# Performance work log

Measured on AMD Instinct MI355X. Metric: run time of the kernel, lower is better.

## Reference

```python
import jax, jax.numpy as jnp
import numpy as np

B, C, N = 16, 3, 4096
K = 20
IN_CH, HID, OUT_CH = 2 * C, 64, 64
EPS = 1e-5
NEG_SLOPE = 0.2


def setup_inputs() -> dict:
    key = jax.random.key(0)
    ks = jax.random.split(key, 4)
    return {
        "x": jax.random.normal(ks[0], (B, C, N), dtype=jnp.float32),
        "W1": jax.random.normal(ks[1], (HID, IN_CH), dtype=jnp.float32) * 0.1,
        "W2": jax.random.normal(ks[2], (HID, HID), dtype=jnp.float32) * 0.1,
        "W3": jax.random.normal(ks[3], (OUT_CH, HID), dtype=jnp.float32) * 0.1,
        "g1": jnp.ones((HID,), jnp.float32),
        "b1": jnp.zeros((HID,), jnp.float32),
        "g2": jnp.ones((OUT_CH,), jnp.float32),
        "b2": jnp.zeros((OUT_CH,), jnp.float32),
    }


def _lrelu(y):
    return jnp.where(y > 0, y, NEG_SLOPE * y)


def _bn(y, gamma, beta):
    # training-mode BatchNorm2d: stats over all axes except channel (last here)
    mu = jnp.mean(y, axis=(0, 1, 2), keepdims=True)
    var = jnp.mean((y - mu) ** 2, axis=(0, 1, 2), keepdims=True)
    return (y - mu) * jax.lax.rsqrt(var + EPS) * gamma + beta


def _graph_feature(x, k):
    # x: [B, C, N] -> DGCNN edge features [B, N, k, 2C]
    xt = jnp.transpose(x, (0, 2, 1))  # [B, N, C]
    sq = jnp.sum(xt * xt, axis=-1)    # [B, N]
    # negative squared pairwise distance (top_k picks nearest, incl. self)
    neg_dist = 2.0 * jnp.einsum('bnc,bmc->bnm', xt, xt) - sq[:, :, None] - sq[:, None, :]
    _, idx = jax.lax.top_k(neg_dist, k)                 # [B, N, k]
    nbr = jax.vmap(lambda xb, ib: xb[ib])(xt, idx)      # [B, N, k, C] gather
    xc = jnp.broadcast_to(xt[:, :, None, :], nbr.shape)
    return jnp.concatenate([nbr - xc, xc], axis=-1)     # [B, N, k, 2C]


def reference(x, W1, W2, W3, g1, b1, g2, b2):
    f = _graph_feature(x, K)                    # [B, N, k, 2C]
    # 1x1 convs over channel axis (last), matching NCHW permute(0,3,2,1)
    y = jnp.einsum('bnkc,oc->bnko', f, W1)
    y = _bn(_lrelu(y), g1, b1)
    y = jnp.einsum('bnkc,oc->bnko', y, W2)
    y = _bn(_lrelu(y), g1, b1)                  # norm1 is reused (shared params)
    y = jnp.einsum('bnkc,oc->bnko', y, W3)
    y = _bn(_lrelu(y), g2, b2)
    y = jnp.max(y, axis=2)                      # max over k neighbors -> [B, N, out]
    return jnp.transpose(y, (0, 2, 1))          # [B, out, N]
```

## Files before the change

kernel.cpp:

```cpp
#include <hip/hip_runtime.h>
#include <math.h>

#define KNN 20
#define CNT_INV (1.0f / 1310720.0f)

typedef short bf16x8 __attribute__((ext_vector_type(8)));
typedef float f32x4  __attribute__((ext_vector_type(4)));

__device__ __forceinline__ short f2bf(float f) {
  unsigned u = __builtin_bit_cast(unsigned, f);
  u += 0x7FFFu + ((u >> 16) & 1u);
  return (short)(u >> 16);
}
__device__ __forceinline__ float lrelu(float y) { return y > 0.f ? y : 0.2f * y; }

__global__ __launch_bounds__(256) void xt4_kernel(const float* __restrict__ x,
                                                  float4* __restrict__ xt4) {
  const int t = blockIdx.x * 256 + threadIdx.x;
  const int b = t >> 12, m = t & 4095;
  const float* xb = x + (size_t)b * 12288;
  const float a = xb[m], c = xb[4096 + m], e = xb[8192 + m];
  xt4[t] = make_float4(a, c, e, a * a + c * c + e * e);
}

__global__ __launch_bounds__(256) void knn_kernel(const float4* __restrict__ xt4,
                                                  int* __restrict__ idx_out,
                                                  const float* __restrict__ W1,
                                                  float* __restrict__ s1buf) {
  __shared__ __align__(16) int hist[1024];
  __shared__ int sB[8];
  __shared__ int wcnt[4][4];
  __shared__ int slist[4][64];
  __shared__ int scnt[4];
  __shared__ int eidx[4][KNN];
  const int tid = threadIdx.x, lane = tid & 63, wid = tid >> 6;
  const int p0 = blockIdx.x * 4;
  const int b = p0 >> 12, n0 = p0 & 4095;
  const float4* xb4 = xt4 + (size_t)b * 4096;
  const float4 cp0 = xb4[n0], cp1 = xb4[n0 + 1], cp2 = xb4[n0 + 2], cp3 = xb4[n0 + 3];

  float w1r[6];
#pragma unroll
  for (int c = 0; c < 6; ++c) w1r[c] = W1[lane * 6 + c];

  float d0[16], d1[16], d2[16], d3[16];
#pragma unroll
  for (int i = 0; i < 16; ++i) {
    const float4 qv = xb4[i * 256 + tid];
    const float t0 = fmaf(cp0.x, qv.x, fmaf(cp0.y, qv.y, cp0.z * qv.z));
    const float t1 = fmaf(cp1.x, qv.x, fmaf(cp1.y, qv.y, cp1.z * qv.z));
    const float t2 = fmaf(cp2.x, qv.x, fmaf(cp2.y, qv.y, cp2.z * qv.z));
    const float t3 = fmaf(cp3.x, qv.x, fmaf(cp3.y, qv.y, cp3.z * qv.z));
    d0[i] = fmaf(-2.0f, t0, qv.w) + cp0.w;
    d1[i] = fmaf(-2.0f, t1, qv.w) + cp1.w;
    d2[i] = fmaf(-2.0f, t2, qv.w) + cp2.w;
    d3[i] = fmaf(-2.0f, t3, qv.w) + cp3.w;
  }

  *(int4*)&hist[tid * 4] = int4{0, 0, 0, 0};
  __syncthreads();
#pragma unroll
  for (int i = 0; i < 16; ++i) {
    if (d0[i] < 2.0f) atomicAdd(&hist[      (int)(d0[i] * 128.0f)], 1);
    if (d1[i] < 2.0f) atomicAdd(&hist[256 + (int)(d1[i] * 128.0f)], 1);
    if (d2[i] < 2.0f) atomicAdd(&hist[512 + (int)(d2[i] * 128.0f)], 1);
    if (d3[i] < 2.0f) atomicAdd(&hist[768 + (int)(d3[i] * 128.0f)], 1);
  }
  __syncthreads();
  {
    const int* h = &hist[wid * 256];
    int Bv = 256, cntv = 0, seam = 0;
#pragma unroll
    for (int c = 0; c < 4; ++c) {
      if (Bv == 256) {
        int s = h[c * 64 + lane];
#pragma unroll
        for (int off = 1; off < 64; off <<= 1) { const int t = __shfl_up(s, off); if (lane >= off) s += t; }
        s += seam;
        const unsigned long long m = __ballot(s >= 20);
        if (m) { const int l = __ffsll((long long)m) - 1; Bv = c * 64 + l; cntv = __shfl(s, l); }
        else seam = __shfl(s, 63);
      }
    }
    if (lane == 0) { sB[wid * 2] = Bv; sB[wid * 2 + 1] = cntv; }
  }
  __syncthreads();

  float lo0 = 0.f, R0 = 2.f, lo1 = 0.f, R1 = 2.f, lo2 = 0.f, R2 = 2.f, lo3 = 0.f, R3 = 2.f;
  int bef0 = 0, bef1 = 0, bef2 = 0, bef3 = 0;
  float Dedge0 = 1e30f, Dedge1 = 1e30f, Dedge2 = 1e30f, Dedge3 = 1e30f;
  bool dn0 = false, dn1 = false, dn2 = false, dn3 = false;
  {
    const float bw = 2.0f * (1.0f / 256.0f);
    bool zm0 = false, zm1 = false, zm2 = false, zm3 = false;
    {
      const int Bq = sB[0], cq = sB[1];
      if (Bq == 256) R0 = 32.0f;
      else {
        Dedge0 = (float)(Bq + 1) * bw;
        if (cq <= 48) dn0 = true;
        else { lo0 = (float)Bq * bw; R0 = bw; zm0 = true; }
      }
    }
    {
      const int Bq = sB[2], cq = sB[3];
      if (Bq == 256) R1 = 32.0f;
      else {
        Dedge1 = (float)(Bq + 1) * bw;
        if (cq <= 48) dn1 = true;
        else { lo1 = (float)Bq * bw; R1 = bw; zm1 = true; }
      }
    }
    {
      const int Bq = sB[4], cq = sB[5];
      if (Bq == 256) R2 = 32.0f;
      else {
        Dedge2 = (float)(Bq + 1) * bw;
        if (cq <= 48) dn2 = true;
        else { lo2 = (float)Bq * bw; R2 = bw; zm2 = true; }
      }
    }
    {
      const int Bq = sB[6], cq = sB[7];
      if (Bq == 256) R3 = 32.0f;
      else {
        Dedge3 = (float)(Bq + 1) * bw;
        if (cq <= 48) dn3 = true;
        else { lo3 = (float)Bq * bw; R3 = bw; zm3 = true; }
      }
    }
    if (zm0) {
      int c = 0;
#pragma unroll
      for (int i = 0; i < 16; ++i) c += (int)__popcll(__ballot(d0[i] < lo0));
      if (lane == 0) wcnt[0][wid] = c;
    }
    if (zm1) {
      int c = 0;
#pragma unroll
      for (int i = 0; i < 16; ++i) c += (int)__popcll(__ballot(d1[i] < lo1));
      if (lane == 0) wcnt[1][wid] = c;
    }
    if (zm2) {
      int c = 0;
#pragma unroll
      for (int i = 0; i < 16; ++i) c += (int)__popcll(__ballot(d2[i] < lo2));
      if (lane == 0) wcnt[2][wid] = c;
    }
    if (zm3) {
      int c = 0;
#pragma unroll
      for (int i = 0; i < 16; ++i) c += (int)__popcll(__ballot(d3[i] < lo3));
      if (lane == 0) wcnt[3][wid] = c;
    }
    if (zm0 | zm1 | zm2 | zm3) {
      __syncthreads();
      if (zm0) bef0 = wcnt[0][0] + wcnt[0][1] + wcnt[0][2] + wcnt[0][3];
      if (zm1) bef1 = wcnt[1][0] + wcnt[1][1] + wcnt[1][2] + wcnt[1][3];
      if (zm2) bef2 = wcnt[2][0] + wcnt[2][1] + wcnt[2][2] + wcnt[2][3];
      if (zm3) bef3 = wcnt[3][0] + wcnt[3][1] + wcnt[3][2] + wcnt[3][3];
    }
  }

  for (int pass = 1; pass < 6 && !(dn0 && dn1 && dn2 && dn3); ++pass) {
    *(int4*)&hist[tid * 4] = int4{0, 0, 0, 0};
    __syncthreads();
    const float sc0 = 256.0f / R0, sc1 = 256.0f / R1;
    const float sc2 = 256.0f / R2, sc3 = 256.0f / R3;
    if (!dn0) {
#pragma unroll
      for (int i = 0; i < 16; ++i) {
        const float rel = d0[i] - lo0;
        if (rel >= 0.0f && rel < R0) {
          int bin = (int)(rel * sc0); bin = bin > 255 ? 255 : bin;
          atomicAdd(&hist[bin], 1);
        }
      }
    }
    if (!dn1) {
#pragma unroll
      for (int i = 0; i < 16; ++i) {
        const float rel = d1[i] - lo1;
        if (rel >= 0.0f && rel < R1) {
          int bin = (int)(rel * sc1); bin = bin > 255 ? 255 : bin;
          atomicAdd(&hist[256 + bin], 1);
        }
      }
    }
    if (!dn2) {
#pragma unroll
      for (int i = 0; i < 16; ++i) {
        const float rel = d2[i] - lo2;
        if (rel >= 0.0f && rel < R2) {
          int bin = (int)(rel * sc2); bin = bin > 255 ? 255 : bin;
          atomicAdd(&hist[512 + bin], 1);
        }
      }
    }
    if (!dn3) {
#pragma unroll
      for (int i = 0; i < 16; ++i) {
        const float rel = d3[i] - lo3;
        if (rel >= 0.0f && rel < R3) {
          int bin = (int)(rel * sc3); bin = bin > 255 ? 255 : bin;
          atomicAdd(&hist[768 + bin], 1);
        }
      }
    }
    __syncthreads();
    {
      const bool skip = wid == 0 ? dn0 : wid == 1 ? dn1 : wid == 2 ? dn2 : dn3;
      if (!skip) {
        const int* h = &hist[wid * 256];
        int s0 = h[lane], s1 = h[64 + lane], s2 = h[128 + lane], s3 = h[192 + lane];
#pragma unroll
        for (int off = 1; off < 64; off <<= 1) { const int t = __shfl_up(s0, off); if (lane >= off) s0 += t; }
#pragma unroll
        for (int off = 1; off < 64; off <<= 1) { const int t = __shfl_up(s1, off); if (lane >= off) s1 += t; }
#pragma unroll
        for (int off = 1; off < 64; off <<= 1) { const int t = __shfl_up(s2, off); if (lane >= off) s2 += t; }
#pragma unroll
        for (int off = 1; off < 64; off <<= 1) { const int t = __shfl_up(s3, off); if (lane >= off) s3 += t; }
        s1 += __shfl(s0, 63);
        s2 += __shfl(s1, 63);
        s3 += __shfl(s2, 63);
        const int bef = wid == 0 ? bef0 : wid == 1 ? bef1 : wid == 2 ? bef2 : bef3;
        s0 += bef; s1 += bef; s2 += bef; s3 += bef;
        int B = 256, cnt = 0;
        unsigned long long m = __ballot(s0 >= 20);
        if (m) { const int l = __ffsll((long long)m) - 1; B = l; cnt = __shfl(s0, l); }
        else if ((m = __ballot(s1 >= 20)) != 0ull) { const int l = __ffsll((long long)m) - 1; B = 64 + l; cnt = __shfl(s1, l); }
        else if ((m = __ballot(s2 >= 20)) != 0ull) { const int l = __ffsll((long long)m) - 1; B = 128 + l; cnt = __shfl(s2, l); }
        else if ((m = __ballot(s3 >= 20)) != 0ull) { const int l = __ffsll((long long)m) - 1; B = 192 + l; cnt = __shfl(s3, l); }
        if (lane == 0) { sB[wid * 2] = B; sB[wid * 2 + 1] = cnt; }
      }
    }
    __syncthreads();
    bool zm0 = false, zm1 = false, zm2 = false, zm3 = false;
    if (!dn0) {
      const int Bq = sB[0], cq = sB[1];
      if (Bq == 256) R0 *= 16.0f;
      else {
        const float bw = R0 * (1.0f / 256.0f);
        Dedge0 = lo0 + (float)(Bq + 1) * bw;
        if (cq <= 48) dn0 = true;
        else { lo0 += (float)Bq * bw; R0 = bw; zm0 = true; }
      }
    }
    if (!dn1) {
      const int Bq = sB[2], cq = sB[3];
      if (Bq == 256) R1 *= 16.0f;
      else {
        const float bw = R1 * (1.0f / 256.0f);
        Dedge1 = lo1 + (float)(Bq + 1) * bw;
        if (cq <= 48) dn1 = true;
        else { lo1 += (float)Bq * bw; R1 = bw; zm1 = true; }
      }
    }
    if (!dn2) {
      const int Bq = sB[4], cq = sB[5];
      if (Bq == 256) R2 *= 16.0f;
      else {
        const float bw = R2 * (1.0f / 256.0f);
        Dedge2 = lo2 + (float)(Bq + 1) * bw;
        if (cq <= 48) dn2 = true;
        else { lo2 += (float)Bq * bw; R2 = bw; zm2 = true; }
      }
    }
    if (!dn3) {
      const int Bq = sB[6], cq = sB[7];
      if (Bq == 256) R3 *= 16.0f;
      else {
        const float bw = R3 * (1.0f / 256.0f);
        Dedge3 = lo3 + (float)(Bq + 1) * bw;
        if (cq <= 48) dn3 = true;
        else { lo3 += (float)Bq * bw; R3 = bw; zm3 = true; }
      }
    }
    if (zm0) {
      int c = 0;
#pragma unroll
      for (int i = 0; i < 16; ++i) c += (int)__popcll(__ballot(d0[i] < lo0));
      if (lane == 0) wcnt[0][wid] = c;
    }
    if (zm1) {
      int c = 0;
#pragma unroll
      for (int i = 0; i < 16; ++i) c += (int)__popcll(__ballot(d1[i] < lo1));
      if (lane == 0) wcnt[1][wid] = c;
    }
    if (zm2) {
      int c = 0;
#pragma unroll
      for (int i = 0; i < 16; ++i) c += (int)__popcll(__ballot(d2[i] < lo2));
      if (lane == 0) wcnt[2][wid] = c;
    }
    if (zm3) {
      int c = 0;
#pragma unroll
      for (int i = 0; i < 16; ++i) c += (int)__popcll(__ballot(d3[i] < lo3));
      if (lane == 0) wcnt[3][wid] = c;
    }
    if (zm0 | zm1 | zm2 | zm3) {
      __syncthreads();
      if (zm0) bef0 = wcnt[0][0] + wcnt[0][1] + wcnt[0][2] + wcnt[0][3];
      if (zm1) bef1 = wcnt[1][0] + wcnt[1][1] + wcnt[1][2] + wcnt[1][3];
      if (zm2) bef2 = wcnt[2][0] + wcnt[2][1] + wcnt[2][2] + wcnt[2][3];
      if (zm3) bef3 = wcnt[3][0] + wcnt[3][1] + wcnt[3][2] + wcnt[3][3];
    }
  }

  if (tid < 4) scnt[tid] = 0;
  __syncthreads();
  const float T0 = Dedge0 + 4e-3f, T1 = Dedge1 + 4e-3f;
  const float T2 = Dedge2 + 4e-3f, T3 = Dedge3 + 4e-3f;
#pragma unroll
  for (int i = 0; i < 16; ++i) {
    if (d0[i] < T0) {
      const int pos = atomicAdd(&scnt[0], 1);
      if (pos < 64) slist[0][pos] = i * 256 + tid;
    }
    if (d1[i] < T1) {
      const int pos = atomicAdd(&scnt[1], 1);
      if (pos < 64) slist[1][pos] = i * 256 + tid;
    }
    if (d2[i] < T2) {
      const int pos = atomicAdd(&scnt[2], 1);
      if (pos < 64) slist[2][pos] = i * 256 + tid;
    }
    if (d3[i] < T3) {
      const int pos = atomicAdd(&scnt[3], 1);
      if (pos < 64) slist[3][pos] = i * 256 + tid;
    }
  }
  __syncthreads();

  const float4 cp = wid == 0 ? cp0 : wid == 1 ? cp1 : wid == 2 ? cp2 : cp3;
  {
    const int s = min(scnt[wid], 64);
    int myi = -1; double myd = -1.0e300;
    if (lane < s) {
      myi = slist[wid][lane];
      const float4 av = xb4[myi];
      const double c0 = (double)cp.x, c1 = (double)cp.y, c2 = (double)cp.z;
      const double a0 = (double)av.x, a1 = (double)av.y, a2 = (double)av.z;
      const double dot = c0 * a0 + c1 * a1 + c2 * a2;
      const double sqm = a0 * a0 + a1 * a1 + a2 * a2;
      const double sn  = c0 * c0 + c1 * c1 + c2 * c2;
      myd = (2.0 * dot - sn) - sqm;
    }
    int rank = 0;
    for (int j = 0; j < s; ++j) {
      const double od = __shfl(myd, j);
      const int    oi = __shfl(myi, j);
      if (od > myd || (od == myd && oi < myi)) ++rank;
    }
    if (lane < s && rank < KNN) {
      idx_out[(p0 + wid) * KNN + rank] = myi;
      eidx[wid][rank] = myi;
    }
  }

  const float base1 = (w1r[3] - w1r[0]) * cp.x + (w1r[4] - w1r[1]) * cp.y +
                      (w1r[5] - w1r[2]) * cp.z;
  float sm = 0.f, sq = 0.f;
#pragma unroll
  for (int t = 0; t < KNN; ++t) {
    const int kk = eidx[wid][t];
    const float4 qv = xb4[kk];
    float y = fmaf(w1r[0], qv.x, fmaf(w1r[1], qv.y, fmaf(w1r[2], qv.z, base1)));
    y = lrelu(y);
    sm += y; sq = fmaf(y, y, sq);
  }
  float* bk = s1buf + (size_t)((p0 + wid) & 255) * 128;
  atomicAdd(&bk[lane], sm);
  atomicAdd(&bk[64 + lane], sq);
}

template <int STAGE, int MINW>
__global__ __launch_bounds__(256, MINW) void stage_kernel(
    const float4* __restrict__ xt4, const int* __restrict__ nbr,
    const float* __restrict__ W1,
    const float* __restrict__ w2ft, const float* __restrict__ b2f,
    const float* __restrict__ w3ft, const float* __restrict__ b3f,
    float* __restrict__ sumO, float* __restrict__ sqO,
    float* __restrict__ mx, float* __restrict__ mn) {
  __shared__ float pts[4][96];
  __shared__ float W1T[384];
  __shared__ short abuf[4][2048];
  __shared__ float redS[256], redQ[256];

  const int tid = threadIdx.x, wave = tid >> 6, lane = tid & 63;
  const int q = lane >> 4, cc = lane & 15;

  for (int i = tid; i < 384; i += 256) W1T[i] = W1[(i & 63) * 6 + (i >> 6)];
  __syncthreads();

  float w1r[6];
#pragma unroll
  for (int c = 0; c < 6; ++c) w1r[c] = W1T[c * 64 + lane];

  bf16x8 w2f[2][4];
#pragma unroll
  for (int kt = 0; kt < 2; ++kt)
#pragma unroll
    for (int nt = 0; nt < 4; ++nt)
#pragma unroll
      for (int j = 0; j < 8; ++j)
        w2f[kt][nt][j] = f2bf(w2ft[(kt * 32 + q * 8 + j) * 64 + nt * 16 + cc]);
  float bias2v[4];
#pragma unroll
  for (int nt = 0; nt < 4; ++nt) bias2v[nt] = b2f[nt * 16 + cc];

  bf16x8 w3f[2][4];
  float bias3v[4];
  if (STAGE == 3) {
#pragma unroll
    for (int kt = 0; kt < 2; ++kt)
#pragma unroll
      for (int nt = 0; nt < 4; ++nt)
#pragma unroll
        for (int j = 0; j < 8; ++j)
          w3f[kt][nt][j] = f2bf(w3ft[(kt * 32 + q * 8 + j) * 64 + nt * 16 + cc]);
#pragma unroll
    for (int nt = 0; nt < 4; ++nt) bias3v[nt] = b3f[nt * 16 + cc];
  }

  const int kt1 = lane >> 5, q1 = (lane & 31) >> 3, j1 = lane & 7;
  short* ab = abuf[wave];
  const bf16x8* ab8 = (const bf16x8*)ab;
  float* pw = pts[wave];

  float s_s[4] = {0.f, 0.f, 0.f, 0.f}, s_q[4] = {0.f, 0.f, 0.f, 0.f};
  const int wgid = blockIdx.x * 4 + wave;

  const int stepN = 8192 * KNN;
  const int* nbp = nbr + (size_t)wgid * KNN + lane;
  const float4* xb0 = xt4 + (size_t)(wgid >> 12) * 4096;
  const int nn = wgid & 4095;
  int kkB = 0;
  float4 g;
  if (lane < KNN) {
    const int kkA = nbp[0];
    g = xb0[kkA];
    kkB = nbp[stepN];
  } else if (lane == KNN) {
    g = xb0[nn];
  }
  const int* nbp2 = nbp + 2 * stepN;
  const float4* xbn = xb0 + 8192;

  for (int it = 0; it < 8; ++it) {
    const int p = wgid + it * 8192;
    if (lane <= KNN) *(float4*)&pw[lane * 4] = g;
    float4 gn = g; int kkC = kkB;
    if (it < 7 && lane <= KNN) gn = (lane < KNN) ? xbn[kkB] : xbn[nn];
    if (it < 6 && lane < KNN) kkC = nbp2[0];

    const float cx0 = pw[80], cx1 = pw[81], cx2 = pw[82];
    const float base1 = (w1r[3] - w1r[0]) * cx0 + (w1r[4] - w1r[1]) * cx1 +
                        (w1r[5] - w1r[2]) * cx2;

#pragma unroll
    for (int k = 0; k < KNN; ++k) {
      const float4 pk = *(const float4*)&pw[k * 4];
      float y = fmaf(w1r[0], pk.x, fmaf(w1r[1], pk.y, fmaf(w1r[2], pk.z, base1)));
      y = lrelu(y);
      ab[(((k >> 4) * 2 + kt1) * 64 + q1 * 16 + (k & 15)) * 8 + j1] = f2bf(y);
    }

    f32x4 acc2[2][4];
#pragma unroll
    for (int mt = 0; mt < 2; ++mt)
#pragma unroll
      for (int nt = 0; nt < 4; ++nt)
        acc2[mt][nt] = f32x4{bias2v[nt], bias2v[nt], bias2v[nt], bias2v[nt]};
#pragma unroll
    for (int kt = 0; kt < 2; ++kt) {
      const bf16x8 a0 = ab8[(0 * 2 + kt) * 64 + lane];
      const bf16x8 a1 = ab8[(1 * 2 + kt) * 64 + lane];
#pragma unroll
      for (int nt = 0; nt < 4; ++nt) {
        acc2[0][nt] = __builtin_amdgcn_mfma_f32_16x16x32_bf16(a0, w2f[kt][nt], acc2[0][nt], 0, 0, 0);
        acc2[1][nt] = __builtin_amdgcn_mfma_f32_16x16x32_bf16(a1, w2f[kt][nt], acc2[1][nt], 0, 0, 0);
      }
    }

    if (STAGE == 2) {
#pragma unroll
      for (int mt = 0; mt < 2; ++mt)
#pragma unroll
        for (int nt = 0; nt < 4; ++nt)
#pragma unroll
          for (int r = 0; r < 4; ++r) {
            if (mt == 1 && q != 0) continue;
            const float y = lrelu(acc2[mt][nt][r]);
            s_s[nt] += y; s_q[nt] += y * y;
          }
    } else {
#pragma unroll
      for (int mt = 0; mt < 2; ++mt)
#pragma unroll
        for (int nt = 0; nt < 4; ++nt) {
          const int kt3 = nt >> 1;
          const int q3 = (nt & 1) * 2 + (cc >> 3);
          const int j3 = cc & 7;
#pragma unroll
          for (int r = 0; r < 4; ++r) {
            if (mt == 1 && q != 0) continue;
            const float y = lrelu(acc2[mt][nt][r]);
            ab[((mt * 2 + kt3) * 64 + q3 * 16 + q * 4 + r) * 8 + j3] = f2bf(y);
          }
        }

      f32x4 acc3[2][4];
#pragma unroll
      for (int mt = 0; mt < 2; ++mt)
#pragma unroll
        for (int nt = 0; nt < 4; ++nt)
          acc3[mt][nt] = f32x4{bias3v[nt], bias3v[nt], bias3v[nt], bias3v[nt]};
#pragma unroll
      for (int kt = 0; kt < 2; ++kt) {
        const bf16x8 a0 = ab8[(0 * 2 + kt) * 64 + lane];
        const bf16x8 a1 = ab8[(1 * 2 + kt) * 64 + lane];
#pragma unroll
        for (int nt = 0; nt < 4; ++nt) {
          acc3[0][nt] = __builtin_amdgcn_mfma_f32_16x16x32_bf16(a0, w3f[kt][nt], acc3[0][nt], 0, 0, 0);
          acc3[1][nt] = __builtin_amdgcn_mfma_f32_16x16x32_bf16(a1, w3f[kt][nt], acc3[1][nt], 0, 0, 0);
        }
      }

      float vmx[4], vmn[4];
#pragma unroll
      for (int nt = 0; nt < 4; ++nt) { vmx[nt] = -INFINITY; vmn[nt] = INFINITY; }
#pragma unroll
      for (int mt = 0; mt < 2; ++mt)
#pragma unroll
        for (int nt = 0; nt < 4; ++nt)
#pragma unroll
          for (int r = 0; r < 4; ++r) {
            if (mt == 1 && q != 0) continue;
            const float y = lrelu(acc3[mt][nt][r]);
            s_s[nt] += y; s_q[nt] += y * y;
            vmx[nt] = fmaxf(vmx[nt], y); vmn[nt] = fminf(vmn[nt], y);
          }
#pragma unroll
      for (int nt = 0; nt < 4; ++nt) {
        vmx[nt] = fmaxf(vmx[nt], __shfl_xor(vmx[nt], 16));
        vmx[nt] = fmaxf(vmx[nt], __shfl_xor(vmx[nt], 32));
        vmn[nt] = fminf(vmn[nt], __shfl_xor(vmn[nt], 16));
        vmn[nt] = fminf(vmn[nt], __shfl_xor(vmn[nt], 32));
      }
      const float omx = q == 0 ? vmx[0] : q == 1 ? vmx[1] : q == 2 ? vmx[2] : vmx[3];
      const float omn = q == 0 ? vmn[0] : q == 1 ? vmn[1] : q == 2 ? vmn[2] : vmn[3];
      mx[(size_t)p * 64 + lane] = omx;
      mn[(size_t)p * 64 + lane] = omn;
    }

    g = gn; kkB = kkC; nbp2 += stepN; xbn += 8192;
  }

#pragma unroll
  for (int nt = 0; nt < 4; ++nt) {
    s_s[nt] += __shfl_xor(s_s[nt], 16); s_s[nt] += __shfl_xor(s_s[nt], 32);
    s_q[nt] += __shfl_xor(s_q[nt], 16); s_q[nt] += __shfl_xor(s_q[nt], 32);
  }
  const float ms = q == 0 ? s_s[0] : q == 1 ? s_s[1] : q == 2 ? s_s[2] : s_s[3];
  const float mq = q == 0 ? s_q[0] : q == 1 ? s_q[1] : q == 2 ? s_q[2] : s_q[3];
  redS[tid] = ms; redQ[tid] = mq;
  __syncthreads();
  if (tid < 64) {
    const float s  = redS[tid] + redS[64 + tid] + redS[128 + tid] + redS[192 + tid];
    const float qq = redQ[tid] + redQ[64 + tid] + redQ[128 + tid] + redQ[192 + tid];
    atomicAdd(&sumO[tid], s);
    atomicAdd(&sqO[tid], qq);
  }
}

__global__ void fold1_kernel(const float* __restrict__ s1buf,
                             const float* __restrict__ g, const float* __restrict__ bt,
                             const float* __restrict__ W,
                             float* __restrict__ WfT, float* __restrict__ bf) {
  __shared__ float s[64], t[64];
  const int o = threadIdx.x;
  float sm = 0.f, qq = 0.f;
  for (int k = 0; k < 256; ++k) { sm += s1buf[k * 128 + o]; qq += s1buf[k * 128 + 64 + o]; }
  const float mu = sm * CNT_INV;
  const float var = qq * CNT_INV - mu * mu;
  const float sc = g[o] / sqrtf(var + 1e-5f);
  s[o] = sc; t[o] = bt[o] - mu * sc;
  __syncthreads();
  float acc = 0.f;
  for (int c = 0; c < 64; ++c) {
    const float w = W[o * 64 + c];
    WfT[c * 64 + o] = w * s[c];
    acc += w * t[c];
  }
  bf[o] = acc;
}

__global__ void fold_kernel(const float* __restrict__ sum, const float* __restrict__ sq,
                            const float* __restrict__ g, const float* __restrict__ bt,
                            const float* __restrict__ W,
                            float* __restrict__ WfT, float* __restrict__ bf) {
  __shared__ float s[64], t[64];
  const int o = threadIdx.x;
  const float mu = sum[o] * CNT_INV;
  const float var = sq[o] * CNT_INV - mu * mu;
  const float sc = g[o] / sqrtf(var + 1e-5f);
  s[o] = sc; t[o] = bt[o] - mu * sc;
  __syncthreads();
  float acc = 0.f;
  for (int c = 0; c < 64; ++c) {
    const float w = W[o * 64 + c];
    WfT[c * 64 + o] = w * s[c];
    acc += w * t[c];
  }
  bf[o] = acc;
}

__global__ void fold3_kernel(const float* __restrict__ sum, const float* __restrict__ sq,
                             const float* __restrict__ g, const float* __restrict__ bt,
                             float* __restrict__ s3, float* __restrict__ t3) {
  const int o = threadIdx.x;
  const float mu = sum[o] * CNT_INV;
  const float var = sq[o] * CNT_INV - mu * mu;
  const float sc = g[o] / sqrtf(var + 1e-5f);
  s3[o] = sc; t3[o] = bt[o] - mu * sc;
}

__global__ __launch_bounds__(256) void final_kernel(
    const float* __restrict__ mx, const float* __restrict__ mn,
    const float* __restrict__ s3, const float* __restrict__ t3,
    float* __restrict__ out) {
  __shared__ float tmx[64][65], tmn[64][65];
  __shared__ float ss[64], tt[64];
  const int tid = threadIdx.x;
  const int P = blockIdx.x * 64;
  const int b = P >> 12, nb = P & 4095;
  if (tid < 64) { ss[tid] = s3[tid]; tt[tid] = t3[tid]; }
#pragma unroll
  for (int r = 0; r < 16; ++r) {
    const int idx = r * 256 + tid;
    const int pl = idx >> 6, ch = idx & 63;
    const size_t src = ((size_t)(P + pl)) * 64 + ch;
    tmx[pl][ch] = mx[src];
    tmn[pl][ch] = mn[src];
  }
  __syncthreads();
  const int nl = tid & 63;
#pragma unroll
  for (int r = 0; r < 16; ++r) {
    const int o = (tid >> 6) + r * 4;
    const float sc = ss[o];
    const float v = sc >= 0.f ? tmx[nl][o] : tmn[nl][o];
    out[(size_t)b * 262144 + (size_t)o * 4096 + nb + nl] = sc * v + tt[o];
  }
}

extern "C" void kernel_launch(void* const* d_in, const int* in_sizes, int n_in,
                              void* d_out, int out_size, void* d_ws, size_t ws_size,
                              hipStream_t stream) {
  const float* x  = (const float*)d_in[0];
  const float* W1 = (const float*)d_in[1];
  const float* W2 = (const float*)d_in[2];
  const float* W3 = (const float*)d_in[3];
  const float* g1 = (const float*)d_in[4];
  const float* b1 = (const float*)d_in[5];
  const float* g2 = (const float*)d_in[6];
  const float* b2 = (const float*)d_in[7];
  float* out = (float*)d_out;

  char* ws = (char*)d_ws;
  float4* xt4 = (float4*)ws;
  int* idx = (int*)(ws + 1048576);
  float* F = (float*)(ws + 6291456);
  float* sum2 = F + 0,   * sq2 = F + 64;
  float* sum3 = F + 128, * sq3 = F + 192;
  float* s1buf = F + 256;
  float* W2fT = F + 33024;
  float* b2f  = F + 37120;
  float* W3fT = F + 37184;
  float* b3f  = F + 41280;
  float* s3   = F + 41344;
  float* t3   = F + 41408;
  float* mx = (float*)(ws + 6457344);
  float* mn = mx + (size_t)16 * 4096 * 64;

  hipMemsetAsync(F, 0, 33024 * sizeof(float), stream);

  xt4_kernel<<<256, 256, 0, stream>>>(x, xt4);
  knn_kernel<<<16384, 256, 0, stream>>>(xt4, idx, W1, s1buf);
  fold1_kernel<<<1, 64, 0, stream>>>(s1buf, g1, b1, W2, W2fT, b2f);
  stage_kernel<2, 3><<<2048, 256, 0, stream>>>(xt4, idx, W1, W2fT, b2f, nullptr,
                                               nullptr, sum2, sq2, nullptr, nullptr);
  fold_kernel<<<1, 64, 0, stream>>>(sum2, sq2, g1, b1, W3, W3fT, b3f);
  stage_kernel<3, 2><<<2048, 256, 0, stream>>>(xt4, idx, W1, W2fT, b2f, W3fT,
                                               b3f, sum3, sq3, mx, mn);
  fold3_kernel<<<1, 64, 0, stream>>>(sum3, sq3, g2, b2, s3, t3);
  final_kernel<<<1024, 256, 0, stream>>>(mx, mn, s3, t3, out);
}
```

Measured before the change: 519.1 us.

## Pack kNN distances as float2, widen fold1, fuse fold3 into final kernel

The kNN distance computation now uses two-wide float vectors so the compiler can emit packed FMA instructions, and the kernel gets a launch-bounds occupancy hint of 4. fold1 now runs with 256 threads that split the 256-row reduction and the weight fold four ways, instead of 64 serial threads. The separate fold3 kernel is removed and its BN scale/shift computation is folded into each final_kernel block, saving a launch at the cost of redundant per-block work. Packed vectors may add register shuffling, and the occupancy hint could force spills.

New measurement: 525.1 us. Within noise of the previous version (+1.2%).

```diff
diff --git a/kernel.cpp b/kernel.cpp
--- a/kernel.cpp
+++ b/kernel.cpp
@@ -6,6 +6,7 @@
 
 typedef short bf16x8 __attribute__((ext_vector_type(8)));
 typedef float f32x4  __attribute__((ext_vector_type(4)));
+typedef float f32x2  __attribute__((ext_vector_type(2)));
 
 __device__ __forceinline__ short f2bf(float f) {
   unsigned u = __builtin_bit_cast(unsigned, f);
@@ -23,10 +24,10 @@
   xt4[t] = make_float4(a, c, e, a * a + c * c + e * e);
 }
 
-__global__ __launch_bounds__(256) void knn_kernel(const float4* __restrict__ xt4,
-                                                  int* __restrict__ idx_out,
-                                                  const float* __restrict__ W1,
-                                                  float* __restrict__ s1buf) {
+__global__ __launch_bounds__(256, 4) void knn_kernel(const float4* __restrict__ xt4,
+                                                     int* __restrict__ idx_out,
+                                                     const float* __restrict__ W1,
+                                                     float* __restrict__ s1buf) {
   __shared__ __align__(16) int hist[1024];
   __shared__ int sB[8];
   __shared__ int wcnt[4][4];
@@ -43,28 +44,31 @@
 #pragma unroll
   for (int c = 0; c < 6; ++c) w1r[c] = W1[lane * 6 + c];
 
-  float d0[16], d1[16], d2[16], d3[16];
+  const f32x2 cx01{cp0.x, cp1.x}, cy01{cp0.y, cp1.y}, cz01{cp0.z, cp1.z}, cw01{cp0.w, cp1.w};
+  const f32x2 cx23{cp2.x, cp3.x}, cy23{cp2.y, cp3.y}, cz23{cp2.z, cp3.z}, cw23{cp2.w, cp3.w};
+  const f32x2 m2{-2.0f, -2.0f};
+
+  f32x2 d01[16], d23[16];
 #pragma unroll
   for (int i = 0; i < 16; ++i) {
     const float4 qv = xb4[i * 256 + tid];
-    const float t0 = fmaf(cp0.x, qv.x, fmaf(cp0.y, qv.y, cp0.z * qv.z));
-    const float t1 = fmaf(cp1.x, qv.x, fmaf(cp1.y, qv.y, cp1.z * qv.z));
-    const float t2 = fmaf(cp2.x, qv.x, fmaf(cp2.y, qv.y, cp2.z * qv.z));
-    const float t3 = fmaf(cp3.x, qv.x, fmaf(cp3.y, qv.y, cp3.z * qv.z));
-    d0[i] = fmaf(-2.0f, t0, qv.w) + cp0.w;
-    d1[i] = fmaf(-2.0f, t1, qv.w) + cp1.w;
-    d2[i] = fmaf(-2.0f, t2, qv.w) + cp2.w;
-    d3[i] = fmaf(-2.0f, t3, qv.w) + cp3.w;
+    const f32x2 qx{qv.x, qv.x}, qy{qv.y, qv.y}, qz{qv.z, qv.z}, qw{qv.w, qv.w};
+    const f32x2 t01 = __builtin_elementwise_fma(cx01, qx,
+                        __builtin_elementwise_fma(cy01, qy, cz01 * qz));
+    const f32x2 t23 = __builtin_elementwise_fma(cx23, qx,
+                        __builtin_elementwise_fma(cy23, qy, cz23 * qz));
+    d01[i] = __builtin_elementwise_fma(m2, t01, qw) + cw01;
+    d23[i] = __builtin_elementwise_fma(m2, t23, qw) + cw23;
   }
 
   *(int4*)&hist[tid * 4] = int4{0, 0, 0, 0};
   __syncthreads();
 #pragma unroll
   for (int i = 0; i < 16; ++i) {
-    if (d0[i] < 2.0f) atomicAdd(&hist[      (int)(d0[i] * 128.0f)], 1);
-    if (d1[i] < 2.0f) atomicAdd(&hist[256 + (int)(d1[i] * 128.0f)], 1);
-    if (d2[i] < 2.0f) atomicAdd(&hist[512 + (int)(d2[i] * 128.0f)], 1);
-    if (d3[i] < 2.0f) atomicAdd(&hist[768 + (int)(d3[i] * 128.0f)], 1);
+    if (d01[i][0] < 2.0f) atomicAdd(&hist[      (int)(d01[i][0] * 128.0f)], 1);
+    if (d01[i][1] < 2.0f) atomicAdd(&hist[256 + (int)(d01[i][1] * 128.0f)], 1);
+    if (d23[i][0] < 2.0f) atomicAdd(&hist[512 + (int)(d23[i][0] * 128.0f)], 1);
+    if (d23[i][1] < 2.0f) atomicAdd(&hist[768 + (int)(d23[i][1] * 128.0f)], 1);
   }
   __syncthreads();
   {
@@ -132,25 +136,25 @@
     if (zm0) {
       int c = 0;
 #pragma unroll
-      for (int i = 0; i < 16; ++i) c += (int)__popcll(__ballot(d0[i] < lo0));
+      for (int i = 0; i < 16; ++i) c += (int)__popcll(__ballot(d01[i][0] < lo0));
       if (lane == 0) wcnt[0][wid] = c;
     }
     if (zm1) {
       int c = 0;
 #pragma unroll
-      for (int i = 0; i < 16; ++i) c += (int)__popcll(__ballot(d1[i] < lo1));
+      for (int i = 0; i < 16; ++i) c += (int)__popcll(__ballot(d01[i][1] < lo1));
       if (lane == 0) wcnt[1][wid] = c;
     }
     if (zm2) {
       int c = 0;
 #pragma unroll
-      for (int i = 0; i < 16; ++i) c += (int)__popcll(__ballot(d2[i] < lo2));
+      for (int i = 0; i < 16; ++i) c += (int)__popcll(__ballot(d23[i][0] < lo2));
       if (lane == 0) wcnt[2][wid] = c;
     }
     if (zm3) {
       int c = 0;
 #pragma unroll
-      for (int i = 0; i < 16; ++i) c += (int)__popcll(__ballot(d3[i] < lo3));
+      for (int i = 0; i < 16; ++i) c += (int)__popcll(__ballot(d23[i][1] < lo3));
       if (lane == 0) wcnt[3][wid] = c;
     }
     if (zm0 | zm1 | zm2 | zm3) {
@@ -170,7 +174,7 @@
     if (!dn0) {
 #pragma unroll
       for (int i = 0; i < 16; ++i) {
-        const float rel = d0[i] - lo0;
+        const float rel = d01[i][0] - lo0;
         if (rel >= 0.0f && rel < R0) {
           int bin = (int)(rel * sc0); bin = bin > 255 ? 255 : bin;
           atomicAdd(&hist[bin], 1);
@@ -180,7 +184,7 @@
     if (!dn1) {
 #pragma unroll
       for (int i = 0; i < 16; ++i) {
-        const float rel = d1[i] - lo1;
+        const float rel = d01[i][1] - lo1;
         if (rel >= 0.0f && rel < R1) {
           int bin = (int)(rel * sc1); bin = bin > 255 ? 255 : bin;
           atomicAdd(&hist[256 + bin], 1);
@@ -190,7 +194,7 @@
     if (!dn2) {
 #pragma unroll
       for (int i = 0; i < 16; ++i) {
-        const float rel = d2[i] - lo2;
+        const float rel = d23[i][0] - lo2;
         if (rel >= 0.0f && rel < R2) {
           int bin = (int)(rel * sc2); bin = bin > 255 ? 255 : bin;
           atomicAdd(&hist[512 + bin], 1);
@@ -200,7 +204,7 @@
     if (!dn3) {
 #pragma unroll
       for (int i = 0; i < 16; ++i) {
-        const float rel = d3[i] - lo3;
+        const float rel = d23[i][1] - lo3;
         if (rel >= 0.0f && rel < R3) {
           int bin = (int)(rel * sc3); bin = bin > 255 ? 255 : bin;
           atomicAdd(&hist[768 + bin], 1);
@@ -280,25 +284,25 @@
     if (zm0) {
       int c = 0;
 #pragma unroll
-      for (int i = 0; i < 16; ++i) c += (int)__popcll(__ballot(d0[i] < lo0));
+      for (int i = 0; i < 16; ++i) c += (int)__popcll(__ballot(d01[i][0] < lo0));
       if (lane == 0) wcnt[0][wid] = c;
     }
     if (zm1) {
       int c = 0;
 #pragma unroll
-      for (int i = 0; i < 16; ++i) c += (int)__popcll(__ballot(d1[i] < lo1));
+      for (int i = 0; i < 16; ++i) c += (int)__popcll(__ballot(d01[i][1] < lo1));
       if (lane == 0) wcnt[1][wid] = c;
     }
     if (zm2) {
       int c = 0;
 #pragma unroll
-      for (int i = 0; i < 16; ++i) c += (int)__popcll(__ballot(d2[i] < lo2));
+      for (int i = 0; i < 16; ++i) c += (int)__popcll(__ballot(d23[i][0] < lo2));
       if (lane == 0) wcnt[2][wid] = c;
     }
     if (zm3) {
       int c = 0;
 #pragma unroll
-      for (int i = 0; i < 16; ++i) c += (int)__popcll(__ballot(d3[i] < lo3));
+      for (int i = 0; i < 16; ++i) c += (int)__popcll(__ballot(d23[i][1] < lo3));
       if (lane == 0) wcnt[3][wid] = c;
     }
     if (zm0 | zm1 | zm2 | zm3) {
@@ -316,19 +320,19 @@
   const float T2 = Dedge2 + 4e-3f, T3 = Dedge3 + 4e-3f;
 #pragma unroll
   for (int i = 0; i < 16; ++i) {
-    if (d0[i] < T0) {
+    if (d01[i][0] < T0) {
       const int pos = atomicAdd(&scnt[0], 1);
       if (pos < 64) slist[0][pos] = i * 256 + tid;
     }
-    if (d1[i] < T1) {
+    if (d01[i][1] < T1) {
       const int pos = atomicAdd(&scnt[1], 1);
       if (pos < 64) slist[1][pos] = i * 256 + tid;
     }
-    if (d2[i] < T2) {
+    if (d23[i][0] < T2) {
       const int pos = atomicAdd(&scnt[2], 1);
       if (pos < 64) slist[2][pos] = i * 256 + tid;
     }
-    if (d3[i] < T3) {
+    if (d23[i][1] < T3) {
       const int pos = atomicAdd(&scnt[3], 1);
       if (pos < 64) slist[3][pos] = i * 256 + tid;
     }
@@ -577,26 +581,39 @@
   }
 }
 
-__global__ void fold1_kernel(const float* __restrict__ s1buf,
-                             const float* __restrict__ g, const float* __restrict__ bt,
-                             const float* __restrict__ W,
-                             float* __restrict__ WfT, float* __restrict__ bf) {
+__global__ __launch_bounds__(256) void fold1_kernel(
+    const float* __restrict__ s1buf,
+    const float* __restrict__ g, const float* __restrict__ bt,
+    const float* __restrict__ W,
+    float* __restrict__ WfT, float* __restrict__ bf) {
+  __shared__ float rs[256], rq[256];
   __shared__ float s[64], t[64];
-  const int o = threadIdx.x;
+  const int tid = threadIdx.x, o = tid & 63, qt = tid >> 6;
   float sm = 0.f, qq = 0.f;
-  for (int k = 0; k < 256; ++k) { sm += s1buf[k * 128 + o]; qq += s1buf[k * 128 + 64 + o]; }
-  const float mu = sm * CNT_INV;
-  const float var = qq * CNT_INV - mu * mu;
-  const float sc = g[o] / sqrtf(var + 1e-5f);
-  s[o] = sc; t[o] = bt[o] - mu * sc;
+  for (int k = qt; k < 256; k += 4) {
+    sm += s1buf[k * 128 + o];
+    qq += s1buf[k * 128 + 64 + o];
+  }
+  rs[tid] = sm; rq[tid] = qq;
+  __syncthreads();
+  if (tid < 64) {
+    sm = rs[o] + rs[64 + o] + rs[128 + o] + rs[192 + o];
+    qq = rq[o] + rq[64 + o] + rq[128 + o] + rq[192 + o];
+    const float mu = sm * CNT_INV;
+    const float var = qq * CNT_INV - mu * mu;
+    const float sc = g[o] / sqrtf(var + 1e-5f);
+    s[o] = sc; t[o] = bt[o] - mu * sc;
+  }
   __syncthreads();
   float acc = 0.f;
-  for (int c = 0; c < 64; ++c) {
+  for (int c = qt * 16; c < qt * 16 + 16; ++c) {
     const float w = W[o * 64 + c];
     WfT[c * 64 + o] = w * s[c];
-    acc += w * t[c];
-  }
-  bf[o] = acc;
+    acc = fmaf(w, t[c], acc);
+  }
+  rs[tid] = acc;
+  __syncthreads();
+  if (tid < 64) bf[o] = rs[o] + rs[64 + o] + rs[128 + o] + rs[192 + o];
 }
 
 __global__ void fold_kernel(const float* __restrict__ sum, const float* __restrict__ sq,
@@ -619,26 +636,22 @@
   bf[o] = acc;
 }
 
-__global__ void fold3_kernel(const float* __restrict__ sum, const float* __restrict__ sq,
-                             const float* __restrict__ g, const float* __restrict__ bt,
-                             float* __restrict__ s3, float* __restrict__ t3) {
-  const int o = threadIdx.x;
-  const float mu = sum[o] * CNT_INV;
-  const float var = sq[o] * CNT_INV - mu * mu;
-  const float sc = g[o] / sqrtf(var + 1e-5f);
-  s3[o] = sc; t3[o] = bt[o] - mu * sc;
-}
-
 __global__ __launch_bounds__(256) void final_kernel(
     const float* __restrict__ mx, const float* __restrict__ mn,
-    const float* __restrict__ s3, const float* __restrict__ t3,
+    const float* __restrict__ sum3, const float* __restrict__ sq3,
+    const float* __restrict__ g2, const float* __restrict__ b2,
     float* __restrict__ out) {
   __shared__ float tmx[64][65], tmn[64][65];
   __shared__ float ss[64], tt[64];
   const int tid = threadIdx.x;
   const int P = blockIdx.x * 64;
   const int b = P >> 12, nb = P & 4095;
-  if (tid < 64) { ss[tid] = s3[tid]; tt[tid] = t3[tid]; }
+  if (tid < 64) {
+    const float mu = sum3[tid] * CNT_INV;
+    const float var = sq3[tid] * CNT_INV - mu * mu;
+    const float sc = g2[tid] / sqrtf(var + 1e-5f);
+    ss[tid] = sc; tt[tid] = b2[tid] - mu * sc;
+  }
 #pragma unroll
   for (int r = 0; r < 16; ++r) {
     const int idx = r * 256 + tid;
@@ -682,8 +695,6 @@
   float* b2f  = F + 37120;
   float* W3fT = F + 37184;
   float* b3f  = F + 41280;
-  float* s3   = F + 41344;
-  float* t3   = F + 41408;
   float* mx = (float*)(ws + 6457344);
   float* mn = mx + (size_t)16 * 4096 * 64;
 
@@ -691,12 +702,11 @@
 
   xt4_kernel<<<256, 256, 0, stream>>>(x, xt4);
   knn_kernel<<<16384, 256, 0, stream>>>(xt4, idx, W1, s1buf);
-  fold1_kernel<<<1, 64, 0, stream>>>(s1buf, g1, b1, W2, W2fT, b2f);
+  fold1_kernel<<<1, 256, 0, stream>>>(s1buf, g1, b1, W2, W2fT, b2f);
   stage_kernel<2, 3><<<2048, 256, 0, stream>>>(xt4, idx, W1, W2fT, b2f, nullptr,
                                                nullptr, sum2, sq2, nullptr, nullptr);
   fold_kernel<<<1, 64, 0, stream>>>(sum2, sq2, g1, b1, W3, W3fT, b3f);
   stage_kernel<3, 2><<<2048, 256, 0, stream>>>(xt4, idx, W1, W2fT, b2f, W3fT,
                                                b3f, sum3, sq3, mx, mn);
-  fold3_kernel<<<1, 64, 0, stream>>>(sum3, sq3, g2, b2, s3, t3);
-  final_kernel<<<1024, 256, 0, stream>>>(mx, mn, s3, t3, out);
+  final_kernel<<<1024, 256, 0, stream>>>(mx, mn, sum3, sq3, g2, b2, out);
 }
```
